# Performance work log

Hardware: AMD Instinct MI355X
Metric: run time of the kernel (lower is better)

The kernel has to match this reference:

```python
import jax, jax.numpy as jnp
import numpy as np

D_MODEL = 1024
EXPAND = 2
HEADDIM = 64
D_STATE = 64
CHUNK = 64
D_INNER = EXPAND * D_MODEL          # 2048
NHEADS = D_INNER // HEADDIM         # 32
D_MLP = int(2.5 * D_MODEL)          # 2560
BATCH = 2
SEQLEN = 4096
PROJ = 2 * D_INNER + 2 * NHEADS * D_STATE + NHEADS + NHEADS * (D_STATE // 2)


def rmsnorm(x, w, eps=1e-5):
    return x * jax.lax.rsqrt(jnp.mean(x * x, axis=-1, keepdims=True) + eps) * w


def apply_rope(x, angles):
    x1 = x[..., 0::2]
    x2 = x[..., 1::2]
    c = jnp.cos(angles)
    s = jnp.sin(angles)
    ev = c * x1 - s * x2
    od = s * x1 + c * x2
    return jnp.stack([ev, od], axis=-1).reshape(x.shape)


def segsum(x):
    # x: (b,h,c,l) -> (b,h,c,l,l); [i,j] = sum_{j<k<=i} x_k (no -inf mask, as in source)
    T = x.shape[-1]
    xx = jnp.broadcast_to(x[..., :, None], x.shape + (T,))
    mask = jnp.tril(jnp.ones((T, T), dtype=bool), -1)
    xx = jnp.where(mask, xx, 0.0)
    return jnp.cumsum(xx, axis=-2)


def ssd(x, A, B, C, chunk):
    # x: (b,s,h,p), A: (b,s,h), B/C: (b,s,h,n); s % chunk == 0
    b, s, h, p = x.shape
    n = B.shape[-1]
    c = s // chunk
    x_c = x.reshape(b, c, chunk, h, p).transpose(0, 1, 3, 2, 4)  # (b,c,h,l,p)
    B_c = B.reshape(b, c, chunk, h, n).transpose(0, 1, 3, 2, 4)  # (b,c,h,l,n)
    C_c = C.reshape(b, c, chunk, h, n).transpose(0, 1, 3, 2, 4)
    A_c = A.reshape(b, c, chunk, h).transpose(0, 1, 3, 2)        # (b,c,h,l)
    A_cum = jnp.cumsum(A_c, axis=-1)
    L = jnp.exp(segsum(A_c.transpose(0, 2, 1, 3))).transpose(0, 2, 1, 3, 4)  # (b,c,h,l,l)
    Bx = jnp.einsum('bchln,bchlp->bchpn', B_c, x_c)
    Y_diag = jnp.einsum('bchln,bchls,bchpn->bchlp', C_c, L, Bx)
    decay_states = jnp.exp(A_cum[..., -1:] - A_cum)
    states = jnp.einsum('bchln,bchl,bchlp->bchpn', B_c, decay_states, x_c)  # (b,c,h,p,n)
    decay_chunk = jnp.exp(A_cum[..., -1])  # (b,c,h)
    h0 = jnp.zeros_like(states[:, 0])

    def step(carry, inp):
        dec, st = inp  # dec: (b,h), st: (b,h,p,n)
        carry = carry * dec[:, :, None, None] + st
        return carry, carry

    _, hs = jax.lax.scan(step, h0, (decay_chunk.transpose(1, 0, 2),
                                    states.transpose(1, 0, 2, 3, 4)))
    final_states = hs.transpose(1, 0, 2, 3, 4)  # (b,c,h,p,n)
    Y_off = jnp.einsum('bchln,bchpn,bchl->bchlp', C_c, final_states, jnp.exp(A_cum))
    Y = (Y_diag + Y_off).transpose(0, 1, 3, 2, 4).reshape(b, s, h * p)
    return Y


def setup_inputs() -> dict:
    key = jax.random.key(0)
    ks = jax.random.split(key, 12)
    sc = 0.02
    return {
        'x': jax.random.normal(ks[0], (BATCH, SEQLEN, D_MODEL), jnp.float32),
        'norm1_w': jnp.ones((D_MODEL,), jnp.float32),
        'norm2_w': jnp.ones((D_MODEL,), jnp.float32),
        'W_in': sc * jax.random.normal(ks[1], (D_MODEL, PROJ), jnp.float32),
        'W_out': sc * jax.random.normal(ks[2], (D_INNER, D_MODEL), jnp.float32),
        'A_log': jax.random.uniform(ks[3], (NHEADS,), jnp.float32, -4.0, -1.0),
        'D_param': jnp.ones((NHEADS,), jnp.float32),
        'dt_bias': jax.random.uniform(ks[4], (NHEADS,), jnp.float32, 0.001, 0.1),
        'B_bias': jnp.ones((1, NHEADS, D_STATE), jnp.float32),
        'C_bias': jnp.ones((1, NHEADS, D_STATE), jnp.float32),
        'Bn_w': jnp.ones((D_STATE,), jnp.float32),
        'Cn_w': jnp.ones((D_STATE,), jnp.float32),
        'Wg': sc * jax.random.normal(ks[5], (D_MODEL, D_MLP), jnp.float32),
        'Wu': sc * jax.random.normal(ks[6], (D_MODEL, D_MLP), jnp.float32),
        'Wd': sc * jax.random.normal(ks[7], (D_MLP, D_MODEL), jnp.float32),
    }


def reference(x, norm1_w, norm2_w, W_in, W_out, A_log, D_param, dt_bias,
              B_bias, C_bias, Bn_w, Cn_w, Wg, Wu, Wd):
    b, s, _ = x.shape
    h = rmsnorm(x, norm1_w)
    proj = h @ W_in
    i = 0
    z = proj[..., i:i + D_INNER]; i += D_INNER
    x_ssm = proj[..., i:i + D_INNER]; i += D_INNER
    B = proj[..., i:i + NHEADS * D_STATE].reshape(b, s, NHEADS, D_STATE); i += NHEADS * D_STATE
    C = proj[..., i:i + NHEADS * D_STATE].reshape(b, s, NHEADS, D_STATE); i += NHEADS * D_STATE
    dt = proj[..., i:i + NHEADS]; i += NHEADS
    theta = proj[..., i:].reshape(b, s, NHEADS, D_STATE // 2)
    dt = jax.nn.softplus(dt + dt_bias)                 # (b,s,h)
    A = -jnp.exp(A_log) * dt
    alpha = jnp.exp(A)
    gamma = (alpha - 1.0) / (A + 1e-6) * 0.5 + 1.0
    B = rmsnorm(B, Bn_w) + B_bias
    C = rmsnorm(C, Cn_w) + C_bias
    cum_theta = jnp.cumsum(dt[..., None] * theta, axis=1)
    B = apply_rope(B, cum_theta)
    C = apply_rope(C, cum_theta)
    x_ssm = x_ssm.reshape(b, s, NHEADS, HEADDIM)
    y = ssd(x_ssm * gamma[..., None], A, B, C, CHUNK)
    skip = jnp.broadcast_to((D_param * x_ssm.sum(-1))[..., None], x_ssm.shape)
    y = y + skip.reshape(b, s, -1)
    y = y * (z * jax.nn.sigmoid(z))
    y = y @ W_out
    x = x + y
    h2 = rmsnorm(x, norm2_w)
    g = h2 @ Wg
    x = x + ((g * jax.nn.sigmoid(g)) * (h2 @ Wu)) @ Wd
    return x
```

## Files before the change

### kernel.cpp

```cpp
#include <hip/hip_runtime.h>
#include <cstdint>
#include <cmath>


typedef __bf16 bf16;
typedef __bf16 bf16x2 __attribute__((ext_vector_type(2)));
typedef __bf16 bf16x4 __attribute__((ext_vector_type(4)));
typedef __bf16 bf16x8 __attribute__((ext_vector_type(8)));
typedef float fx4 __attribute__((ext_vector_type(4)));

#define DEV __device__ __forceinline__

#define OFF_PROJ    0ull
#define OFF_HHI     134217728ull
#define OFF_HLO     150994944ull
#define OFF_WTIN    167772160ull
#define OFF_WTHI    184549376ull
#define OFF_WTLO    186908672ull
#define OFF_PROJT   189267968ull
#define OFF_BX      189267968ull
#define OFF_STATES  222822400ull
#define OFF_WTOUT   222822400ull
#define OFF_WTGU    227016704ull
#define OFF_WTD     237502464ull
#define OFF_ABUF    256376832ull
#define OFF_XSUM    257425408ull
#define OFF_ROWSUM  258473984ull
#define OFF_EXPA    260571136ull
#define OFF_DCHUNK  262668288ull
#define OFF_GAMMA   262684672ull
#define WS_NEEDED   263733248ull

#define OFF_MBF     83886080ull

DEV void async_copy16(void* lds, const void* gptr) {
  __builtin_amdgcn_global_load_lds(
      (const __attribute__((address_space(1))) unsigned int*)(gptr),
      (__attribute__((address_space(3))) unsigned int*)(lds),
      16, 0, 0);
}

DEV float warp_sum64(float v) {
  #pragma unroll
  for (int o = 32; o; o >>= 1) v += __shfl_xor(v, o);
  return v;
}

DEV float red16(float v) {
  v += __shfl_xor(v, 1); v += __shfl_xor(v, 2);
  v += __shfl_xor(v, 4); v += __shfl_xor(v, 8);
  return v;
}

DEV float softplus_f(float x) { return x > 20.f ? x : log1pf(expf(x)); }
DEV float sigmoid_f(float x) { return 1.f / (1.f + expf(-x)); }

__global__ __launch_bounds__(256) void transpose_cast(
    const float* __restrict__ src, int ld, int col0,
    bf16* __restrict__ dst, int R, int C)
{
  __shared__ float tile[32][33];
  const int c0 = blockIdx.x * 32, r0 = blockIdx.y * 32;
  const int tx = threadIdx.x & 31, ty = threadIdx.x >> 5;
  #pragma unroll
  for (int ii = 0; ii < 4; ++ii) {
    int i = ty + ii * 8;
    int c = c0 + tx;
    tile[i][tx] = (c < C) ? src[(size_t)(r0 + i) * ld + col0 + c] : 0.f;
  }
  __syncthreads();
  #pragma unroll
  for (int ii = 0; ii < 4; ++ii) {
    int i = ty + ii * 8;
    dst[(size_t)(c0 + i) * R + r0 + tx] = (bf16)tile[tx][i];
  }
}

__global__ __launch_bounds__(256) void transpose_cast_hilo(
    const float* __restrict__ src, int ld, int col0,
    bf16* __restrict__ dhi, bf16* __restrict__ dlo, int R, int C)
{
  __shared__ float tile[32][33];
  const int c0 = blockIdx.x * 32, r0 = blockIdx.y * 32;
  const int tx = threadIdx.x & 31, ty = threadIdx.x >> 5;
  #pragma unroll
  for (int ii = 0; ii < 4; ++ii) {
    int i = ty + ii * 8;
    int c = c0 + tx;
    tile[i][tx] = (c < C) ? src[(size_t)(r0 + i) * ld + col0 + c] : 0.f;
  }
  __syncthreads();
  #pragma unroll
  for (int ii = 0; ii < 4; ++ii) {
    int i = ty + ii * 8;
    float v = tile[tx][i];
    bf16 hi = (bf16)v;
    size_t o = (size_t)(c0 + i) * R + r0 + tx;
    dhi[o] = hi;
    dlo[o] = (bf16)(v - (float)hi);
  }
}

__global__ __launch_bounds__(256) void rmsnorm_kernel(
    const float* __restrict__ x, const float* __restrict__ w,
    bf16* __restrict__ hi, bf16* __restrict__ lo)
{
  __shared__ float red[4];
  const size_t row = blockIdx.x;
  const int tid = threadIdx.x;
  float4 v = ((const float4*)(x + row * 1024))[tid];
  float ss = v.x * v.x + v.y * v.y + v.z * v.z + v.w * v.w;
  ss = warp_sum64(ss);
  if ((tid & 63) == 0) red[tid >> 6] = ss;
  __syncthreads();
  float tot = red[0] + red[1] + red[2] + red[3];
  float s = rsqrtf(tot * (1.f / 1024.f) + 1e-5f);
  float4 wv = ((const float4*)w)[tid];
  float h0 = v.x * s * wv.x, h1 = v.y * s * wv.y, h2 = v.z * s * wv.z, h3 = v.w * s * wv.w;
  bf16x4 hv = { (bf16)h0, (bf16)h1, (bf16)h2, (bf16)h3 };
  *(bf16x4*)(hi + row * 1024 + tid * 4) = hv;
  if (lo) {
    bf16x4 lv = { (bf16)(h0 - (float)hv[0]), (bf16)(h1 - (float)hv[1]),
                  (bf16)(h2 - (float)hv[2]), (bf16)(h3 - (float)hv[3]) };
    *(bf16x4*)(lo + row * 1024 + tid * 4) = lv;
  }
}

__global__ __launch_bounds__(256) void gemm_tail(
    const bf16* Ahi, const bf16* Alo, const bf16* Whi, const bf16* Wlo,
    float* Cout)
{
  __shared__ bf16 Ah[128 * 64], Al[128 * 64], Bh[128 * 64], Bl[128 * 64];
  const int tid = threadIdx.x, wid = tid >> 6, lane = tid & 63;
  const int m0 = blockIdx.y * 128, n0 = blockIdx.x * 128;
  const int wm = (wid & 1) * 64, wn = (wid >> 1) * 64;
  fx4 acc[4][4];
  #pragma unroll
  for (int i = 0; i < 4; ++i)
    #pragma unroll
    for (int j = 0; j < 4; ++j) { fx4 z = {0.f, 0.f, 0.f, 0.f}; acc[i][j] = z; }

  const int srow = wid * 32 + (lane >> 3);
  const int slot = lane & 7;

  for (int k0 = 0; k0 < 1024; k0 += 64) {
    __syncthreads();
    #pragma unroll
    for (int i = 0; i < 4; ++i) {
      int m = srow + i * 8;
      int cA = ((slot ^ (m & 7)) * 8);
      size_t ao = (size_t)(m0 + m) * 1024 + k0 + cA;
      async_copy16(&Ah[wid * 2048 + i * 512], Ahi + ao);
      async_copy16(&Al[wid * 2048 + i * 512], Alo + ao);
      int n = srow + i * 8;
      int cB = ((slot ^ (n & 7)) * 8);
      size_t bo = (size_t)(n0 + n) * 1024 + k0 + cB;
      async_copy16(&Bh[wid * 2048 + i * 512], Whi + bo);
      async_copy16(&Bl[wid * 2048 + i * 512], Wlo + bo);
    }
    __syncthreads();
    #pragma unroll
    for (int kk = 0; kk < 2; ++kk) {
      bf16x8 ah[4], al[4], bh[4], bl[4];
      #pragma unroll
      for (int i = 0; i < 4; ++i) {
        int mm = wm + i * 16 + (lane & 15);
        int sA = (kk * 4 + (lane >> 4)) ^ (mm & 7);
        ah[i] = *(const bf16x8*)&Ah[mm * 64 + sA * 8];
        al[i] = *(const bf16x8*)&Al[mm * 64 + sA * 8];
        int nn = wn + i * 16 + (lane & 15);
        int sB = (kk * 4 + (lane >> 4)) ^ (nn & 7);
        bh[i] = *(const bf16x8*)&Bh[nn * 64 + sB * 8];
        bl[i] = *(const bf16x8*)&Bl[nn * 64 + sB * 8];
      }
      #pragma unroll
      for (int i = 0; i < 4; ++i)
        #pragma unroll
        for (int j = 0; j < 4; ++j) {
          acc[i][j] = __builtin_amdgcn_mfma_f32_16x16x32_bf16(ah[i], bh[j], acc[i][j], 0, 0, 0);
          acc[i][j] = __builtin_amdgcn_mfma_f32_16x16x32_bf16(ah[i], bl[j], acc[i][j], 0, 0, 0);
          acc[i][j] = __builtin_amdgcn_mfma_f32_16x16x32_bf16(al[i], bh[j], acc[i][j], 0, 0, 0);
        }
    }
  }
  const int r0 = (lane >> 4) * 4, cc = lane & 15;
  #pragma unroll
  for (int i = 0; i < 4; ++i)
    #pragma unroll
    for (int j = 0; j < 4; ++j)
      #pragma unroll
      for (int r = 0; r < 4; ++r) {
        int m = m0 + wm + i * 16 + r0 + r;
        int n = n0 + wn + j * 16 + cc;
        Cout[(size_t)m * 1152 + n] = acc[i][j][r];
      }
}

__global__ __launch_bounds__(256) void dt_kernel(
    float* projT, const float* __restrict__ A_log, const float* __restrict__ dt_bias,
    float* __restrict__ a_buf, float* __restrict__ gamma_buf)
{
  const int idx = blockIdx.x * 256 + threadIdx.x;
  const int t = idx >> 5, h = idx & 31;
  float dtr = projT[(size_t)t * 1152 + h] + dt_bias[h];
  float dt = softplus_f(dtr);
  float a = -expf(A_log[h]) * dt;
  float alpha = expf(a);
  float gamma = (alpha - 1.f) / (a + 1e-6f) * 0.5f + 1.f;
  projT[(size_t)t * 1152 + h] = dt;
  a_buf[idx] = a;
  gamma_buf[idx] = gamma;
}

__global__ __launch_bounds__(512, 2) void gemm_proj256(
    const bf16* __restrict__ A, const bf16* __restrict__ B, bf16* __restrict__ Cout,
    const float* __restrict__ gamma_buf, float* __restrict__ xsum,
    const float* __restrict__ Bn_w, const float* __restrict__ Cn_w,
    const float* __restrict__ B_bias, const float* __restrict__ C_bias)
{
  __shared__ bf16 lds[65536];
  const int tid = threadIdx.x, wid = tid >> 6, lane = tid & 63;
  const int bid = blockIdx.x;
  const int swz = (bid & 7) * 128 + (bid >> 3);
  const int by = swz >> 5, bx = swz & 31;
  const int m0 = by * 256, n0 = bx * 256;
  const int wr = wid >> 2, wc = wid & 3;
  const int fl = lane & 15, fq = lane >> 4;
  const int rloc = wid * 8 + (lane >> 3);
  const int colSwz = ((lane & 7) ^ (lane >> 3)) * 8;

  fx4 acc[8][4];
  #pragma unroll
  for (int i = 0; i < 8; ++i)
    #pragma unroll
    for (int j = 0; j < 4; ++j) { fx4 z = {0.f, 0.f, 0.f, 0.f}; acc[i][j] = z; }

  const bf16* gA = A + (size_t)(m0 + rloc) * 1024 + colSwz;
  const bf16* gB = B + (size_t)(n0 + rloc) * 1024 + colSwz;

  auto STAGE = [&](int u, int h) {
    const bf16* s = (h < 2) ? gB : gA;
    s += (size_t)(h & 1) * 128 * 1024 + u * 64;
    bf16* d = &lds[((u & 1) * 4 + h) * 8192 + wid * 512];
    async_copy16(d, s);
    async_copy16(d + 4096, s + 64 * 1024);
  };

  STAGE(0, 0); STAGE(0, 1); STAGE(0, 2); STAGE(0, 3);
  STAGE(1, 0); STAGE(1, 1);
  asm volatile("s_waitcnt vmcnt(4)" ::: "memory");
  __builtin_amdgcn_s_barrier();

  const int NT = 16;
  bf16x8 bfrag[4][2];
  for (int t = 0; t < NT; ++t) {
    const int Bb = (t & 1) * 32768;
    const int Ab = Bb + 16384;
    #pragma unroll
    for (int p = 0; p < 4; ++p) {
      bf16x8 af[2][2];
      if (p == 0) {
        #pragma unroll
        for (int j = 0; j < 4; ++j) {
          int nn = wc * 64 + j * 16 + fl;
          #pragma unroll
          for (int kk = 0; kk < 2; ++kk) {
            int q = (kk * 4 + fq) ^ (nn & 7);
            bfrag[j][kk] = *(const bf16x8*)&lds[Bb + nn * 64 + q * 8];
          }
        }
      }
      #pragma unroll
      for (int ii = 0; ii < 2; ++ii) {
        int mm = wr * 128 + (p * 2 + ii) * 16 + fl;
        #pragma unroll
        for (int kk = 0; kk < 2; ++kk) {
          int q = (kk * 4 + fq) ^ (mm & 7);
          af[ii][kk] = *(const bf16x8*)&lds[Ab + mm * 64 + q * 8];
        }
      }
      {
        int H = 4 * t + 6 + p;
        if (H < 4 * NT) STAGE(H >> 2, H & 3);
      }
      if (p == 3) {
        if (t == NT - 2) asm volatile("s_waitcnt vmcnt(0)" ::: "memory");
        else             asm volatile("s_waitcnt vmcnt(4)" ::: "memory");
      }
      __builtin_amdgcn_s_barrier();
      asm volatile("s_waitcnt lgkmcnt(0)" ::: "memory");
      __builtin_amdgcn_sched_barrier(0);
      __builtin_amdgcn_s_setprio(1);
      #pragma unroll
      for (int ii = 0; ii < 2; ++ii)
        #pragma unroll
        for (int j = 0; j < 4; ++j)
          #pragma unroll
          for (int kk = 0; kk < 2; ++kk)
            acc[p * 2 + ii][j] = __builtin_amdgcn_mfma_f32_16x16x32_bf16(
                af[ii][kk], bfrag[j][kk], acc[p * 2 + ii][j], 0, 0, 0);
      __builtin_amdgcn_s_setprio(0);
      __builtin_amdgcn_s_barrier();
    }
  }

  const int reg = bx >> 3;
  const int hh = ((n0 + wc * 64) & 2047) >> 6;
  const int mwb = m0 + wr * 128;
  const int nwb = n0 + wc * 64;
  if (reg == 0) {
    #pragma unroll
    for (int i = 0; i < 8; ++i)
      #pragma unroll
      for (int j = 0; j < 4; ++j)
        #pragma unroll
        for (int r = 0; r < 4; ++r) {
          int m = mwb + i * 16 + fq * 4 + r;
          int n = nwb + j * 16 + fl;
          Cout[(size_t)m * 8192 + n] = (bf16)acc[i][j][r];
        }
  } else if (reg == 1) {
    #pragma unroll
    for (int i = 0; i < 8; ++i)
      #pragma unroll
      for (int r = 0; r < 4; ++r) {
        float s = acc[i][0][r] + acc[i][1][r] + acc[i][2][r] + acc[i][3][r];
        s = red16(s);
        int m = mwb + i * 16 + fq * 4 + r;
        if (fl == 0) xsum[(size_t)m * 32 + hh] = s;
        float g = gamma_buf[(size_t)m * 32 + hh];
        #pragma unroll
        for (int j = 0; j < 4; ++j) {
          int n = nwb + j * 16 + fl;
          Cout[(size_t)m * 8192 + n] = (bf16)(acc[i][j][r] * g);
        }
      }
  } else {
    const float* w = (reg == 2) ? Bn_w : Cn_w;
    const float* bias = (reg == 2) ? B_bias : C_bias;
    #pragma unroll
    for (int i = 0; i < 8; ++i)
      #pragma unroll
      for (int r = 0; r < 4; ++r) {
        float ss = acc[i][0][r] * acc[i][0][r] + acc[i][1][r] * acc[i][1][r]
                 + acc[i][2][r] * acc[i][2][r] + acc[i][3][r] * acc[i][3][r];
        ss = red16(ss);
        float sc = rsqrtf(ss * (1.f / 64.f) + 1e-5f);
        int m = mwb + i * 16 + fq * 4 + r;
        #pragma unroll
        for (int j = 0; j < 4; ++j) {
          int c = j * 16 + fl;
          Cout[(size_t)m * 8192 + nwb + c] =
              (bf16)(acc[i][j][r] * sc * w[c] + bias[hh * 64 + c]);
        }
      }
  }
}

template <int MODE>
__global__ __launch_bounds__(512, 2) void gemm128x256(
    const bf16* __restrict__ A, const bf16* __restrict__ B, void* __restrict__ Cout,
    const float* __restrict__ resid, int NT, int lda, int ldc, int nbx)
{
  __shared__ bf16 lds[49152];
  const int tid = threadIdx.x, wid = tid >> 6, lane = tid & 63;
  const int cpx = gridDim.x >> 3;
  const int bid = blockIdx.x;
  const int swz = (bid & 7) * cpx + (bid >> 3);
  const int by = swz / nbx, bx = swz - by * nbx;
  const int m0 = by * 128, n0 = bx * 256;
  const int wr = wid >> 2, wc = wid & 3;
  const int fl = lane & 15, fq = lane >> 4;
  const int rloc = wid * 8 + (lane >> 3);
  const int colSwz = ((lane & 7) ^ (lane >> 3)) * 8;
  const int K = NT * 64;

  fx4 acc[4][4];
  #pragma unroll
  for (int i = 0; i < 4; ++i)
    #pragma unroll
    for (int j = 0; j < 4; ++j) { fx4 z = {0.f, 0.f, 0.f, 0.f}; acc[i][j] = z; }

  const bf16* gA = A + (size_t)(m0 + rloc) * lda + colSwz;
  const bf16* gB = B + (size_t)(n0 + rloc) * K + colSwz;

  auto STAGE = [&](int u, int h) {
    const bf16* s;
    size_t str;
    if (h < 2) { s = gB + (size_t)h * 128 * K; str = (size_t)K; }
    else       { s = gA;                       str = (size_t)lda; }
    s += u * 64;
    bf16* d = &lds[((u & 1) * 3 + h) * 8192 + wid * 512];
    async_copy16(d, s);
    async_copy16(d + 4096, s + 64 * str);
  };

  STAGE(0, 0); STAGE(0, 1); STAGE(0, 2);
  STAGE(1, 0); STAGE(1, 1);
  asm volatile("s_waitcnt vmcnt(4)" ::: "memory");
  __builtin_amdgcn_s_barrier();

  bf16x8 bfrag[4][2];
  for (int t = 0; t < NT; ++t) {
    const int base = (t & 1) * 24576;
    #pragma unroll
    for (int p = 0; p < 4; ++p) {
      bf16x8 af[2];
      if (p == 0) {
        #pragma unroll
        for (int j = 0; j < 4; ++j) {
          int nn = wc * 64 + j * 16 + fl;
          #pragma unroll
          for (int kk = 0; kk < 2; ++kk) {
            int q = (kk * 4 + fq) ^ (nn & 7);
            bfrag[j][kk] = *(const bf16x8*)&lds[base + (nn >> 7) * 8192 + (nn & 127) * 64 + q * 8];
          }
        }
      }
      {
        int mm = wr * 64 + p * 16 + fl;
        #pragma unroll
        for (int kk = 0; kk < 2; ++kk) {
          int q = (kk * 4 + fq) ^ (mm & 7);
          af[kk] = *(const bf16x8*)&lds[base + 2 * 8192 + mm * 64 + q * 8];
        }
      }
      if (p == 0)      { if (t + 1 < NT) STAGE(t + 1, 2); }
      else if (p == 1) { if (t + 2 < NT) STAGE(t + 2, 0); }
      else if (p == 2) { if (t + 2 < NT) STAGE(t + 2, 1); }
      if (p == 3) {
        if (t == NT - 2) asm volatile("s_waitcnt vmcnt(0)" ::: "memory");
        else             asm volatile("s_waitcnt vmcnt(4)" ::: "memory");
      }
      __builtin_amdgcn_s_barrier();
      asm volatile("s_waitcnt lgkmcnt(0)" ::: "memory");
      __builtin_amdgcn_sched_barrier(0);
      __builtin_amdgcn_s_setprio(1);
      #pragma unroll
      for (int j = 0; j < 4; ++j)
        #pragma unroll
        for (int kk = 0; kk < 2; ++kk)
          acc[p][j] = __builtin_amdgcn_mfma_f32_16x16x32_bf16(
              af[kk], bfrag[j][kk], acc[p][j], 0, 0, 0);
      __builtin_amdgcn_s_setprio(0);
      __builtin_amdgcn_s_barrier();
    }
  }

  const int mwb = m0 + wr * 64;
  const int nwb = n0 + wc * 64;
  #pragma unroll
  for (int i = 0; i < 4; ++i)
    #pragma unroll
    for (int j = 0; j < 4; ++j)
      #pragma unroll
      for (int r = 0; r < 4; ++r) {
        int m = mwb + i * 16 + fq * 4 + r;
        int n = nwb + j * 16 + fl;
        size_t off = (size_t)m * ldc + n;
        float v = acc[i][j][r];
        if (MODE == 1) ((bf16*)Cout)[off] = (bf16)v;
        else ((float*)Cout)[off] = v + resid[off];
      }
}

__global__ __launch_bounds__(512, 2) void gemm_gusilu(
    const bf16* __restrict__ A, const bf16* __restrict__ B,
    bf16* __restrict__ Mout, int nbx)
{
  __shared__ bf16 lds[49152];
  const int tid = threadIdx.x, wid = tid >> 6, lane = tid & 63;
  const int cpx = gridDim.x >> 3;
  const int bid = blockIdx.x;
  const int swz = (bid & 7) * cpx + (bid >> 3);
  const int by = swz / nbx, bx = swz - by * nbx;
  const int m0 = by * 128, n0 = bx * 128;
  const int ws = wid >> 2;
  const int wr = (wid >> 1) & 1, wc = wid & 1;
  const int fl = lane & 15, fq = lane >> 4;
  const int rloc = wid * 8 + (lane >> 3);
  const int colSwz = ((lane & 7) ^ (lane >> 3)) * 8;
  const int NT = 16, K = 1024;

  fx4 acc[4][4];
  #pragma unroll
  for (int i = 0; i < 4; ++i)
    #pragma unroll
    for (int j = 0; j < 4; ++j) { fx4 z = {0.f, 0.f, 0.f, 0.f}; acc[i][j] = z; }

  const bf16* gA  = A + (size_t)(m0 + rloc) * K + colSwz;
  const bf16* gBg = B + (size_t)(n0 + rloc) * K + colSwz;
  const bf16* gBu = B + (size_t)(2560 + n0 + rloc) * K + colSwz;

  auto STAGE = [&](int u, int h) {
    const bf16* s = (h == 0) ? gBg : (h == 1) ? gBu : gA;
    s += u * 64;
    bf16* d = &lds[((u & 1) * 3 + h) * 8192 + wid * 512];
    async_copy16(d, s);
    async_copy16(d + 4096, s + 64 * K);
  };

  STAGE(0, 0); STAGE(0, 1); STAGE(0, 2);
  STAGE(1, 0); STAGE(1, 1);
  asm volatile("s_waitcnt vmcnt(4)" ::: "memory");
  __builtin_amdgcn_s_barrier();

  bf16x8 bfrag[4][2];
  for (int t = 0; t < NT; ++t) {
    const int base = (t & 1) * 24576;
    #pragma unroll
    for (int p = 0; p < 4; ++p) {
      bf16x8 af[2];
      if (p == 0) {
        #pragma unroll
        for (int j = 0; j < 4; ++j) {
          int nn = wc * 64 + j * 16 + fl;
          #pragma unroll
          for (int kk = 0; kk < 2; ++kk) {
            int q = (kk * 4 + fq) ^ (nn & 7);
            bfrag[j][kk] = *(const bf16x8*)&lds[base + ws * 8192 + nn * 64 + q * 8];
          }
        }
      }
      {
        int mm = wr * 64 + p * 16 + fl;
        #pragma unroll
        for (int kk = 0; kk < 2; ++kk) {
          int q = (kk * 4 + fq) ^ (mm & 7);
          af[kk] = *(const bf16x8*)&lds[base + 2 * 8192 + mm * 64 + q * 8];
        }
      }
      if (p == 0)      { if (t + 1 < NT) STAGE(t + 1, 2); }
      else if (p == 1) { if (t + 2 < NT) STAGE(t + 2, 0); }
      else if (p == 2) { if (t + 2 < NT) STAGE(t + 2, 1); }
      if (p == 3) {
        if (t == NT - 2) asm volatile("s_waitcnt vmcnt(0)" ::: "memory");
        else             asm volatile("s_waitcnt vmcnt(4)" ::: "memory");
      }
      __builtin_amdgcn_s_barrier();
      asm volatile("s_waitcnt lgkmcnt(0)" ::: "memory");
      __builtin_amdgcn_sched_barrier(0);
      __builtin_amdgcn_s_setprio(1);
      #pragma unroll
      for (int j = 0; j < 4; ++j)
        #pragma unroll
        for (int kk = 0; kk < 2; ++kk)
          acc[p][j] = __builtin_amdgcn_mfma_f32_16x16x32_bf16(
              af[kk], bfrag[j][kk], acc[p][j], 0, 0, 0);
      __builtin_amdgcn_s_setprio(0);
      __builtin_amdgcn_s_barrier();
    }
  }

  float* uex = (float*)lds;
  if (ws == 1) {
    #pragma unroll
    for (int i = 0; i < 4; ++i)
      #pragma unroll
      for (int j = 0; j < 4; ++j)
        #pragma unroll
        for (int r = 0; r < 4; ++r) {
          int row = wr * 64 + i * 16 + fq * 4 + r;
          int col = wc * 64 + j * 16 + fl;
          uex[row * 132 + col] = acc[i][j][r];
        }
  }
  __syncthreads();
  if (ws == 0) {
    #pragma unroll
    for (int i = 0; i < 4; ++i)
      #pragma unroll
      for (int j = 0; j < 4; ++j)
        #pragma unroll
        for (int r = 0; r < 4; ++r) {
          int row = wr * 64 + i * 16 + fq * 4 + r;
          int col = wc * 64 + j * 16 + fl;
          float g = acc[i][j][r];
          float u = uex[row * 132 + col];
          Mout[(size_t)(m0 + row) * 2560 + n0 + col] =
              (bf16)(g * sigmoid_f(g) * u);
        }
  }
}

__global__ __launch_bounds__(256) void chunk_sum_kernel(
    const float* __restrict__ projT, float* __restrict__ S)
{
  __shared__ float lds[8 * 288];
  const int blk = blockIdx.x;
  const int hq = blockIdx.y;
  const size_t row0 = (size_t)blk * 64;
  const int tid = threadIdx.x;
  float s = 0.f;
  #pragma unroll 1
  for (int batch = 0; batch < 8; ++batch) {
    __syncthreads();
    const float* src = projT + (row0 + batch * 8) * 1152;
    #pragma unroll
    for (int i = 0; i < 9; ++i) {
      int idx = i * 256 + tid;
      int r = idx / 288, col = idx - r * 288;
      int gcol = (col < 32) ? col : (32 + hq * 256 + (col - 32));
      lds[idx] = src[r * 1152 + gcol];
    }
    __syncthreads();
    int hl = tid >> 5, d = tid & 31;
    #pragma unroll
    for (int r = 0; r < 8; ++r)
      s += lds[r * 288 + hq * 8 + hl] * lds[r * 288 + 32 + hl * 32 + d];
  }
  S[(size_t)blk * 1024 + hq * 256 + tid] = s;
}

__global__ __launch_bounds__(256) void rope_kernel(
    bf16* proj, const float* __restrict__ projT, const float* __restrict__ S)
{
  __shared__ float angs[64 * 33], angc[64 * 33];
  const int blk = blockIdx.x;
  const int b = blk >> 11, c = (blk >> 5) & 63, h = blk & 31;
  const size_t t0 = (size_t)b * 4096 + c * 64;
  const int w = threadIdx.x >> 6, lane = threadIdx.x & 63;
  const float* tr = projT + (t0 + lane) * 1152;
  float dtv = tr[h];
  const float* thp = tr + 32 + h * 32 + w * 8;
  float4 th0 = *(const float4*)thp;
  float4 th1 = *(const float4*)(thp + 4);
  const float* Sp = S + (size_t)(b * 64 + lane) * 1024 + h * 32 + w * 8;
  float4 S0 = *(const float4*)Sp;
  float4 S1 = *(const float4*)(Sp + 4);
  float th[8] = { th0.x, th0.y, th0.z, th0.w, th1.x, th1.y, th1.z, th1.w };
  float Sv[8] = { S0.x, S0.y, S0.z, S0.w, S1.x, S1.y, S1.z, S1.w };
  #pragma unroll 1
  for (int j = 0; j < 8; ++j) {
    int d = w * 8 + j;
    float sv = (lane < c) ? Sv[j] : 0.f;
    float off = warp_sum64(sv);
    float v = dtv * th[j];
    #pragma unroll
    for (int o = 1; o < 64; o <<= 1) { float u = __shfl_up(v, o); if (lane >= o) v += u; }
    float ang = off + v;
    float sn, cs;
    sincosf(ang, &sn, &cs);
    angs[lane * 33 + d] = sn;
    angc[lane * 33 + d] = cs;
  }
  __syncthreads();
  const int tt = threadIdx.x >> 2, q = threadIdx.x & 3;
  const size_t base = (t0 + tt) * 8192 + 4096 + h * 64 + q * 16;
  #pragma unroll
  for (int m = 0; m < 2; ++m) {
    bf16* p = proj + base + m * 2048;
    bf16x8 v0 = *(const bf16x8*)(p);
    bf16x8 v1 = *(const bf16x8*)(p + 8);
    bf16x8 r0, r1;
    #pragma unroll
    for (int pp = 0; pp < 4; ++pp) {
      int d = q * 8 + pp;
      float e1 = (float)v0[2 * pp], e2 = (float)v0[2 * pp + 1];
      float sn = angs[tt * 33 + d], cs = angc[tt * 33 + d];
      r0[2 * pp]     = (bf16)(cs * e1 - sn * e2);
      r0[2 * pp + 1] = (bf16)(sn * e1 + cs * e2);
    }
    #pragma unroll
    for (int pp = 0; pp < 4; ++pp) {
      int d = q * 8 + 4 + pp;
      float e1 = (float)v1[2 * pp], e2 = (float)v1[2 * pp + 1];
      float sn = angs[tt * 33 + d], cs = angc[tt * 33 + d];
      r1[2 * pp]     = (bf16)(cs * e1 - sn * e2);
      r1[2 * pp + 1] = (bf16)(sn * e1 + cs * e2);
    }
    *(bf16x8*)(p) = r0;
    *(bf16x8*)(p + 8) = r1;
  }
}

__global__ __launch_bounds__(256) void ssd1_kernel(
    const bf16* __restrict__ proj, const float* __restrict__ a_buf,
    bf16* __restrict__ Bx, bf16* __restrict__ states,
    float* __restrict__ rowsum, float* __restrict__ expac, float* __restrict__ dchunk)
{
  __shared__ bf16 Xs[64 * 72], Bs[64 * 72];
  __shared__ float acum[64], dsv[64];
  const int blk = blockIdx.x;
  const int h = blk & 31;
  const size_t bs0 = ((size_t)(blk >> 5)) * 64;
  const int tid = threadIdx.x;
  const int l = tid >> 2, p0 = (tid & 3) * 16;
  {
    const bf16* xrow = proj + (bs0 + l) * 8192 + 2048 + h * 64 + p0;
    *(bf16x8*)&Xs[l * 72 + p0]     = ((const bf16x8*)xrow)[0];
    *(bf16x8*)&Xs[l * 72 + p0 + 8] = ((const bf16x8*)xrow)[1];
    const bf16* brow = proj + (bs0 + l) * 8192 + 4096 + h * 64 + p0;
    *(bf16x8*)&Bs[l * 72 + p0]     = ((const bf16x8*)brow)[0];
    *(bf16x8*)&Bs[l * 72 + p0 + 8] = ((const bf16x8*)brow)[1];
  }
  if (tid < 64) {
    float v = a_buf[(bs0 + tid) * 32 + h];
    #pragma unroll
    for (int o = 1; o < 64; o <<= 1) { float u = __shfl_up(v, o); if (tid >= o) v += u; }
    acum[tid] = v;
    float a63 = __shfl(v, 63);
    dsv[tid] = expf(a63 - v);
    expac[(size_t)blk * 64 + tid] = expf(v);
    if (tid == 63) dchunk[blk] = expf(v);
  }
  __syncthreads();
  {
    float al = acum[l];
    float rs = 0.f;
    for (int s = tid & 3; s <= l; s += 4) rs += expf(al - acum[s]);
    rs += __shfl_xor(rs, 1);
    rs += __shfl_xor(rs, 2);
    if ((tid & 3) == 0) rowsum[(size_t)blk * 64 + l] = rs + (float)(63 - l);
  }
  const int wv = tid >> 6, lane = tid & 63;
  const int mi = lane & 15, kq = lane >> 4;
  const int m0 = wv * 16;
  fx4 accB[4], accS[4];
  #pragma unroll
  for (int j4 = 0; j4 < 4; ++j4) { fx4 z = {0.f,0.f,0.f,0.f}; accB[j4] = z; accS[j4] = z; }
  #pragma unroll
  for (int kk = 0; kk < 2; ++kk) {
    const int lb = kk * 32 + kq * 8;
    bf16x8 aX, aXd;
    #pragma unroll
    for (int j = 0; j < 8; ++j) {
      bf16 xv = Xs[(lb + j) * 72 + m0 + mi];
      aX[j] = xv;
      aXd[j] = (bf16)((float)xv * dsv[lb + j]);
    }
    #pragma unroll
    for (int j4 = 0; j4 < 4; ++j4) {
      bf16x8 bB;
      #pragma unroll
      for (int j = 0; j < 8; ++j) bB[j] = Bs[(lb + j) * 72 + j4 * 16 + mi];
      accB[j4] = __builtin_amdgcn_mfma_f32_16x16x32_bf16(aX, bB, accB[j4], 0, 0, 0);
      accS[j4] = __builtin_amdgcn_mfma_f32_16x16x32_bf16(aXd, bB, accS[j4], 0, 0, 0);
    }
  }
  const size_t obase = (size_t)blk * 4096;
  #pragma unroll
  for (int j4 = 0; j4 < 4; ++j4) {
    #pragma unroll
    for (int r = 0; r < 4; ++r) {
      int p = m0 + kq * 4 + r;
      int n = j4 * 16 + mi;
      Bx[obase + p * 64 + n] = (bf16)accB[j4][r];
      states[obase + p * 64 + n] = (bf16)accS[j4][r];
    }
  }
}

__global__ __launch_bounds__(128) void ssd2_kernel(
    bf16* __restrict__ states, const float* __restrict__ dchunk)
{
  const int blk = blockIdx.x;
  const int b = blk >> 9, rest = blk & 511;
  const int h = rest >> 4, q = rest & 15;
  const int e0 = q * 256 + threadIdx.x * 2;
  float fs0 = 0.f, fs1 = 0.f;
  #pragma unroll 2
  for (int c = 0; c < 64; ++c) {
    size_t idx = ((size_t)(b * 2048 + c * 32 + h) * 4096) + e0;
    float dec = dchunk[b * 2048 + c * 32 + h];
    bf16x2 st = *(const bf16x2*)(states + idx);
    fs0 = fs0 * dec + (float)st[0];
    fs1 = fs1 * dec + (float)st[1];
    bf16x2 o = { (bf16)fs0, (bf16)fs1 };
    *(bf16x2*)(states + idx) = o;
  }
}

__global__ __launch_bounds__(256) void ssd3_kernel(
    bf16* proj, const bf16* __restrict__ Bx, const bf16* __restrict__ FS,
    const float* __restrict__ rowsum, const float* __restrict__ expac,
    const float* __restrict__ xsum, const float* __restrict__ D_param)
{
  __shared__ bf16 Cs[64 * 72], BxS[64 * 72], FSs[64 * 72];
  __shared__ float rs_s[64], ea_s[64], sk_s[64];
  const int blk = blockIdx.x;
  const int h = blk & 31;
  const size_t bs0 = ((size_t)(blk >> 5)) * 64;
  const int tid = threadIdx.x;
  const int l = tid >> 2, q0 = (tid & 3) * 16;
  {
    const bf16* crow = proj + (bs0 + l) * 8192 + 6144 + h * 64 + q0;
    *(bf16x8*)&Cs[l * 72 + q0]     = ((const bf16x8*)crow)[0];
    *(bf16x8*)&Cs[l * 72 + q0 + 8] = ((const bf16x8*)crow)[1];
    size_t mb = (size_t)blk * 4096 + l * 64 + q0;
    *(bf16x8*)&BxS[l * 72 + q0]     = ((const bf16x8*)(Bx + mb))[0];
    *(bf16x8*)&BxS[l * 72 + q0 + 8] = ((const bf16x8*)(Bx + mb))[1];
    *(bf16x8*)&FSs[l * 72 + q0]     = ((const bf16x8*)(FS + mb))[0];
    *(bf16x8*)&FSs[l * 72 + q0 + 8] = ((const bf16x8*)(FS + mb))[1];
  }
  if (tid < 64) {
    rs_s[tid] = rowsum[(size_t)blk * 64 + tid];
    ea_s[tid] = expac[(size_t)blk * 64 + tid];
    sk_s[tid] = D_param[h] * xsum[(bs0 + tid) * 32 + h];
  }
  __syncthreads();
  const int wv = tid >> 6, lane = tid & 63;
  const int mi = lane & 15, kq = lane >> 4;
  const int m0 = wv * 16;
  fx4 acc1[4], acc2[4];
  #pragma unroll
  for (int j4 = 0; j4 < 4; ++j4) { fx4 z = {0.f,0.f,0.f,0.f}; acc1[j4] = z; acc2[j4] = z; }
  #pragma unroll
  for (int kk = 0; kk < 2; ++kk) {
    bf16x8 aC = *(const bf16x8*)&Cs[(m0 + mi) * 72 + kk * 32 + kq * 8];
    #pragma unroll
    for (int j4 = 0; j4 < 4; ++j4) {
      bf16x8 bx = *(const bf16x8*)&BxS[(j4 * 16 + mi) * 72 + kk * 32 + kq * 8];
      bf16x8 fs = *(const bf16x8*)&FSs[(j4 * 16 + mi) * 72 + kk * 32 + kq * 8];
      acc1[j4] = __builtin_amdgcn_mfma_f32_16x16x32_bf16(aC, bx, acc1[j4], 0, 0, 0);
      acc2[j4] = __builtin_amdgcn_mfma_f32_16x16x32_bf16(aC, fs, acc2[j4], 0, 0, 0);
    }
  }
  #pragma unroll
  for (int j4 = 0; j4 < 4; ++j4) {
    #pragma unroll
    for (int r = 0; r < 4; ++r) {
      int li = m0 + kq * 4 + r;
      int p = j4 * 16 + mi;
      float y = rs_s[li] * acc1[j4][r] + ea_s[li] * acc2[j4][r] + sk_s[li];
      size_t zoff = (bs0 + li) * 8192 + h * 64 + p;
      float z = (float)proj[zoff];
      proj[zoff + 2048] = (bf16)(y * z * sigmoid_f(z));
    }
  }
}

extern "C" void kernel_launch(void* const* d_in, const int* in_sizes, int n_in,
                              void* d_out, int out_size, void* d_ws, size_t ws_size,
                              hipStream_t stream) {
  (void)in_sizes; (void)n_in; (void)out_size;
  if (ws_size < WS_NEEDED) return;
  const float* x       = (const float*)d_in[0];
  const float* n1w     = (const float*)d_in[1];
  const float* n2w     = (const float*)d_in[2];
  const float* W_in    = (const float*)d_in[3];
  const float* W_out   = (const float*)d_in[4];
  const float* A_log   = (const float*)d_in[5];
  const float* D_param = (const float*)d_in[6];
  const float* dt_bias = (const float*)d_in[7];
  const float* B_bias  = (const float*)d_in[8];
  const float* C_bias  = (const float*)d_in[9];
  const float* Bn_w    = (const float*)d_in[10];
  const float* Cn_w    = (const float*)d_in[11];
  const float* Wg      = (const float*)d_in[12];
  const float* Wu      = (const float*)d_in[13];
  const float* Wd      = (const float*)d_in[14];
  float* out = (float*)d_out;
  char* ws = (char*)d_ws;

  bf16*  proj   = (bf16*)(ws + OFF_PROJ);
  float* projT  = (float*)(ws + OFF_PROJT);
  bf16*  h_hi   = (bf16*)(ws + OFF_HHI);
  bf16*  h_lo   = (bf16*)(ws + OFF_HLO);
  bf16*  Wt_in  = (bf16*)(ws + OFF_WTIN);
  bf16*  Wt_hi  = (bf16*)(ws + OFF_WTHI);
  bf16*  Wt_lo  = (bf16*)(ws + OFF_WTLO);
  bf16*  Wt_out = (bf16*)(ws + OFF_WTOUT);
  bf16*  Wt_gu  = (bf16*)(ws + OFF_WTGU);
  bf16*  Wt_d   = (bf16*)(ws + OFF_WTD);
  bf16*  Bx     = (bf16*)(ws + OFF_BX);
  bf16*  states = (bf16*)(ws + OFF_STATES);
  float* a_buf  = (float*)(ws + OFF_ABUF);
  float* xsum_  = (float*)(ws + OFF_XSUM);
  float* rowsum = (float*)(ws + OFF_ROWSUM);
  float* expac  = (float*)(ws + OFF_EXPA);
  float* dchunk = (float*)(ws + OFF_DCHUNK);
  float* gamma_ = (float*)(ws + OFF_GAMMA);
  float* Ssum   = (float*)(ws + OFF_HLO);
  bf16*  ybf    = proj + 2048;
  bf16*  mbf    = (bf16*)(ws + OFF_MBF);
  bf16*  h2bf   = h_hi;
  float* x2     = out;

  transpose_cast<<<dim3(256, 32), 256, 0, stream>>>(W_in, 9248, 0, Wt_in, 1024, 8192);
  transpose_cast_hilo<<<dim3(36, 32), 256, 0, stream>>>(W_in, 9248, 8192, Wt_hi, Wt_lo, 1024, 1056);

  rmsnorm_kernel<<<8192, 256, 0, stream>>>(x, n1w, h_hi, h_lo);

  gemm_tail<<<dim3(9, 64), 256, 0, stream>>>(h_hi, h_lo, Wt_hi, Wt_lo, projT);
  dt_kernel<<<1024, 256, 0, stream>>>(projT, A_log, dt_bias, a_buf, gamma_);
  gemm_proj256<<<dim3(1024), 512, 0, stream>>>(h_hi, Wt_in, proj, gamma_, xsum_,
                                               Bn_w, Cn_w, B_bias, C_bias);

  chunk_sum_kernel<<<dim3(128, 4), 256, 0, stream>>>(projT, Ssum);
  rope_kernel<<<4096, 256, 0, stream>>>(proj, projT, Ssum);

  ssd1_kernel<<<4096, 256, 0, stream>>>(proj, a_buf, Bx, states, rowsum, expac, dchunk);
  ssd2_kernel<<<1024, 128, 0, stream>>>(states, dchunk);
  ssd3_kernel<<<4096, 256, 0, stream>>>(proj, Bx, states, rowsum, expac, xsum_, D_param);

  transpose_cast<<<dim3(32, 64), 256, 0, stream>>>(W_out, 1024, 0, Wt_out, 2048, 1024);
  transpose_cast<<<dim3(80, 32), 256, 0, stream>>>(Wg, 2560, 0, Wt_gu, 1024, 2560);
  transpose_cast<<<dim3(80, 32), 256, 0, stream>>>(Wu, 2560, 0, Wt_gu + (size_t)2560 * 1024, 1024, 2560);
  transpose_cast<<<dim3(32, 80), 256, 0, stream>>>(Wd, 1024, 0, Wt_d, 2560, 1024);

  gemm128x256<2><<<dim3(256), 512, 0, stream>>>(ybf, Wt_out, x2, x, 32, 8192, 1024, 4);

  rmsnorm_kernel<<<8192, 256, 0, stream>>>(x2, n2w, h2bf, nullptr);
  gemm_gusilu<<<dim3(1280), 512, 0, stream>>>(h2bf, Wt_gu, mbf, 20);
  gemm128x256<2><<<dim3(256), 512, 0, stream>>>(mbf, Wt_d, out, x2, 40, 2560, 1024, 4);
}
```

Baseline: 741.8 us.

## Widen gemm_tail N tile to 192 and fuse dt/gamma epilogue into it

The tail GEMM tile changes from 128x128 to 128x192, so the 1152-wide output needs 6 column blocks instead of 9 and each A tile is reused across more columns. The separate dt_kernel is removed: the softplus, decay and gamma computation for the first 32 columns now runs in the GEMM epilogue, which saves one launch and a read-modify-write pass over projT. In exchange each thread holds more accumulator registers (24 fx4), the launch bounds request 2 blocks per CU, and the grid shrinks to 384 blocks, which may leave part of the GPU idle.

New measurement: 737.3 us, median of 2. No clear change (-0.6%).

```diff
diff --git a/kernel.cpp b/kernel.cpp
--- a/kernel.cpp
+++ b/kernel.cpp
@@ -126,57 +126,65 @@
   }
 }
 
-__global__ __launch_bounds__(256) void gemm_tail(
+__global__ __launch_bounds__(256, 2) void gemm_tail(
     const bf16* Ahi, const bf16* Alo, const bf16* Whi, const bf16* Wlo,
-    float* Cout)
-{
-  __shared__ bf16 Ah[128 * 64], Al[128 * 64], Bh[128 * 64], Bl[128 * 64];
+    float* Cout,
+    const float* __restrict__ A_log, const float* __restrict__ dt_bias,
+    float* __restrict__ a_buf, float* __restrict__ gamma_buf)
+{
+  __shared__ bf16 Ah[128 * 64], Al[128 * 64];
+  __shared__ bf16 Bh[192 * 64], Bl[192 * 64];
   const int tid = threadIdx.x, wid = tid >> 6, lane = tid & 63;
-  const int m0 = blockIdx.y * 128, n0 = blockIdx.x * 128;
-  const int wm = (wid & 1) * 64, wn = (wid >> 1) * 64;
-  fx4 acc[4][4];
+  const int m0 = blockIdx.y * 128, n0 = blockIdx.x * 192;
+  const int wm = (wid & 1) * 64, wn = (wid >> 1) * 96;
+  fx4 acc[4][6];
   #pragma unroll
   for (int i = 0; i < 4; ++i)
     #pragma unroll
-    for (int j = 0; j < 4; ++j) { fx4 z = {0.f, 0.f, 0.f, 0.f}; acc[i][j] = z; }
-
-  const int srow = wid * 32 + (lane >> 3);
+    for (int j = 0; j < 6; ++j) { fx4 z = {0.f, 0.f, 0.f, 0.f}; acc[i][j] = z; }
+
+  const int rsub = lane >> 3;
   const int slot = lane & 7;
+  const int colSwz = ((slot ^ rsub) * 8);
 
   for (int k0 = 0; k0 < 1024; k0 += 64) {
     __syncthreads();
     #pragma unroll
     for (int i = 0; i < 4; ++i) {
-      int m = srow + i * 8;
-      int cA = ((slot ^ (m & 7)) * 8);
-      size_t ao = (size_t)(m0 + m) * 1024 + k0 + cA;
-      async_copy16(&Ah[wid * 2048 + i * 512], Ahi + ao);
-      async_copy16(&Al[wid * 2048 + i * 512], Alo + ao);
-      int n = srow + i * 8;
-      int cB = ((slot ^ (n & 7)) * 8);
-      size_t bo = (size_t)(n0 + n) * 1024 + k0 + cB;
-      async_copy16(&Bh[wid * 2048 + i * 512], Whi + bo);
-      async_copy16(&Bl[wid * 2048 + i * 512], Wlo + bo);
+      int row = i * 32 + wid * 8 + rsub;
+      size_t ao = (size_t)(m0 + row) * 1024 + k0 + colSwz;
+      async_copy16(&Ah[i * 2048 + wid * 512], Ahi + ao);
+      async_copy16(&Al[i * 2048 + wid * 512], Alo + ao);
+    }
+    #pragma unroll
+    for (int i = 0; i < 6; ++i) {
+      int row = i * 32 + wid * 8 + rsub;
+      size_t bo = (size_t)(n0 + row) * 1024 + k0 + colSwz;
+      async_copy16(&Bh[i * 2048 + wid * 512], Whi + bo);
+      async_copy16(&Bl[i * 2048 + wid * 512], Wlo + bo);
     }
     __syncthreads();
     #pragma unroll
     for (int kk = 0; kk < 2; ++kk) {
-      bf16x8 ah[4], al[4], bh[4], bl[4];
+      bf16x8 ah[4], al[4], bh[6], bl[6];
       #pragma unroll
       for (int i = 0; i < 4; ++i) {
         int mm = wm + i * 16 + (lane & 15);
         int sA = (kk * 4 + (lane >> 4)) ^ (mm & 7);
         ah[i] = *(const bf16x8*)&Ah[mm * 64 + sA * 8];
         al[i] = *(const bf16x8*)&Al[mm * 64 + sA * 8];
-        int nn = wn + i * 16 + (lane & 15);
+      }
+      #pragma unroll
+      for (int j = 0; j < 6; ++j) {
+        int nn = wn + j * 16 + (lane & 15);
         int sB = (kk * 4 + (lane >> 4)) ^ (nn & 7);
-        bh[i] = *(const bf16x8*)&Bh[nn * 64 + sB * 8];
-        bl[i] = *(const bf16x8*)&Bl[nn * 64 + sB * 8];
+        bh[j] = *(const bf16x8*)&Bh[nn * 64 + sB * 8];
+        bl[j] = *(const bf16x8*)&Bl[nn * 64 + sB * 8];
       }
       #pragma unroll
       for (int i = 0; i < 4; ++i)
         #pragma unroll
-        for (int j = 0; j < 4; ++j) {
+        for (int j = 0; j < 6; ++j) {
           acc[i][j] = __builtin_amdgcn_mfma_f32_16x16x32_bf16(ah[i], bh[j], acc[i][j], 0, 0, 0);
           acc[i][j] = __builtin_amdgcn_mfma_f32_16x16x32_bf16(ah[i], bl[j], acc[i][j], 0, 0, 0);
           acc[i][j] = __builtin_amdgcn_mfma_f32_16x16x32_bf16(al[i], bh[j], acc[i][j], 0, 0, 0);
@@ -187,29 +195,23 @@
   #pragma unroll
   for (int i = 0; i < 4; ++i)
     #pragma unroll
-    for (int j = 0; j < 4; ++j)
+    for (int j = 0; j < 6; ++j)
       #pragma unroll
       for (int r = 0; r < 4; ++r) {
         int m = m0 + wm + i * 16 + r0 + r;
         int n = n0 + wn + j * 16 + cc;
-        Cout[(size_t)m * 1152 + n] = acc[i][j][r];
-      }
-}
-
-__global__ __launch_bounds__(256) void dt_kernel(
-    float* projT, const float* __restrict__ A_log, const float* __restrict__ dt_bias,
-    float* __restrict__ a_buf, float* __restrict__ gamma_buf)
-{
-  const int idx = blockIdx.x * 256 + threadIdx.x;
-  const int t = idx >> 5, h = idx & 31;
-  float dtr = projT[(size_t)t * 1152 + h] + dt_bias[h];
-  float dt = softplus_f(dtr);
-  float a = -expf(A_log[h]) * dt;
-  float alpha = expf(a);
-  float gamma = (alpha - 1.f) / (a + 1e-6f) * 0.5f + 1.f;
-  projT[(size_t)t * 1152 + h] = dt;
-  a_buf[idx] = a;
-  gamma_buf[idx] = gamma;
+        float v = acc[i][j][r];
+        if (n < 32) {
+          float dt = softplus_f(v + dt_bias[n]);
+          float a = -expf(A_log[n]) * dt;
+          float alpha = expf(a);
+          float gamma = (alpha - 1.f) / (a + 1e-6f) * 0.5f + 1.f;
+          a_buf[(size_t)m * 32 + n] = a;
+          gamma_buf[(size_t)m * 32 + n] = gamma;
+          v = dt;
+        }
+        Cout[(size_t)m * 1152 + n] = v;
+      }
 }
 
 __global__ __launch_bounds__(512, 2) void gemm_proj256(
@@ -882,8 +884,8 @@
 
   rmsnorm_kernel<<<8192, 256, 0, stream>>>(x, n1w, h_hi, h_lo);
 
-  gemm_tail<<<dim3(9, 64), 256, 0, stream>>>(h_hi, h_lo, Wt_hi, Wt_lo, projT);
-  dt_kernel<<<1024, 256, 0, stream>>>(projT, A_log, dt_bias, a_buf, gamma_);
+  gemm_tail<<<dim3(6, 64), 256, 0, stream>>>(h_hi, h_lo, Wt_hi, Wt_lo, projT,
+                                             A_log, dt_bias, a_buf, gamma_);
   gemm_proj256<<<dim3(1024), 512, 0, stream>>>(h_hi, Wt_in, proj, gamma_, xsum_,
                                                Bn_w, Cn_w, B_bias, C_bias);
 
```
